# Kernel tuning notes

Hardware: AMD Instinct MI355X
Metric: run time of the kernel (lower is better)

The kernel has to match this reference:

```python
import jax, jax.numpy as jnp
import numpy as np

N_NODES = 100000
N_EDGES = 640000
NUM_GRAPHS = 128
NUM_FEATURES = 128
HIDDEN = 16
NUM_CLASSES = 10


def setup_inputs() -> dict:
    key = jax.random.key(0)
    ks = jax.random.split(key, 9)
    x = jax.random.normal(ks[0], (N_NODES, NUM_FEATURES), dtype=jnp.float32)
    edge_index = jax.random.randint(ks[1], (2, N_EDGES), 0, N_NODES, dtype=jnp.int64)
    batch = jnp.sort(jax.random.randint(ks[2], (N_NODES,), 0, NUM_GRAPHS, dtype=jnp.int64))
    W1 = jax.random.normal(ks[3], (NUM_FEATURES, HIDDEN), dtype=jnp.float32) * 0.1
    b1 = jax.random.normal(ks[4], (HIDDEN,), dtype=jnp.float32) * 0.1
    W2 = jax.random.normal(ks[5], (HIDDEN, HIDDEN), dtype=jnp.float32) * 0.1
    b2 = jax.random.normal(ks[6], (HIDDEN,), dtype=jnp.float32) * 0.1
    Wfc = jax.random.normal(ks[7], (HIDDEN, NUM_CLASSES), dtype=jnp.float32) * 0.1
    bfc = jax.random.normal(ks[8], (NUM_CLASSES,), dtype=jnp.float32) * 0.1
    return {"x": x, "edge_index": edge_index, "batch": batch,
            "W1": W1, "b1": b1, "W2": W2, "b2": b2, "Wfc": Wfc, "bfc": bfc}


def reference(x, edge_index, batch, W1, b1, W2, b2, Wfc, bfc):
    src, dst = edge_index[0], edge_index[1]

    def gin_layer(h, W, b):
        # GINConv (eps=0): nn((1+eps)*x_i + sum_{j in N(i)} x_j)
        agg = jax.ops.segment_sum(h[src], dst, num_segments=N_NODES)
        return jax.nn.relu((h + agg) @ W + b)

    h = gin_layer(x, W1, b1)   # [N, 16]
    h = gin_layer(h, W2, b2)   # [N, 16]

    # global mean pool over graphs
    sums = jax.ops.segment_sum(h, batch, num_segments=NUM_GRAPHS)        # [G, 16]
    counts = jax.ops.segment_sum(jnp.ones((N_NODES,), h.dtype), batch,
                                 num_segments=NUM_GRAPHS)                # [G]
    pooled = sums / jnp.maximum(counts, 1.0)[:, None]
    return pooled @ Wfc + bfc  # [G, num_classes]
```

## Files before the change

### kernel.cpp

```cpp
#include <hip/hip_runtime.h>
#include <hip/hip_bf16.h>

#define N_NODES   100000
#define N_EDGES   640000
#define NUM_GRAPHS 128
#define NUM_FEAT  128
#define HIDDEN    16
#define NUM_CLS   10

#define NBLK   256
#define EPB    (N_EDGES / NBLK)
#define NBUCK  256
#define BSHIFT 9
#define BNODES 512

#define MM1_ROWS 64
__global__ __launch_bounds__(256) void k_mm1_bcount(const float* __restrict__ x,
                                                    const float* __restrict__ W1,
                                                    float* __restrict__ y,
                                                    const int* __restrict__ ei,
                                                    int* __restrict__ cnt,
                                                    int N, int gridMM1) {
    __shared__ float sx[MM1_ROWS][132];
    __shared__ float sw[NUM_FEAT * HIDDEN];
    const int t = threadIdx.x;

    if (blockIdx.x >= gridMM1) {
        int* h = (int*)&sx[0][0];
        const int b = blockIdx.x - gridMM1;
        h[t] = 0;
        __syncthreads();
        const int e0 = b * EPB, e1 = e0 + EPB;
        for (int e = e0 + t; e < e1; e += 256)
            atomicAdd(&h[ei[N_EDGES + e] >> BSHIFT], 1);
        __syncthreads();
        cnt[b * NBUCK + t] = h[t];
        return;
    }

    const int rowbase = blockIdx.x * MM1_ROWS;
    const int nrows = min(MM1_ROWS, N - rowbase);

    for (int i = t; i < NUM_FEAT * HIDDEN; i += 256) sw[i] = W1[i];

    for (int i = t; i < nrows * 32; i += 256) {
        int r = i >> 5, q = i & 31;
        float4 v = ((const float4*)(x + (size_t)(rowbase + r) * NUM_FEAT))[q];
        *(float4*)&sx[r][q * 4] = v;
    }
    __syncthreads();

    const int r  = t >> 2;
    const int c0 = (t & 3) * 4;
    if (r < nrows) {
        float4 o = {0.f, 0.f, 0.f, 0.f};
        #pragma unroll 4
        for (int k4 = 0; k4 < 32; ++k4) {
            float4 xv = *(const float4*)&sx[r][k4 * 4];
            const float* wb = &sw[(k4 * 4) * HIDDEN + c0];
            float4 w0 = *(const float4*)(wb);
            float4 w1 = *(const float4*)(wb + HIDDEN);
            float4 w2 = *(const float4*)(wb + 2 * HIDDEN);
            float4 w3 = *(const float4*)(wb + 3 * HIDDEN);
            o.x += xv.x * w0.x + xv.y * w1.x + xv.z * w2.x + xv.w * w3.x;
            o.y += xv.x * w0.y + xv.y * w1.y + xv.z * w2.y + xv.w * w3.y;
            o.z += xv.x * w0.z + xv.y * w1.z + xv.z * w2.z + xv.w * w3.z;
            o.w += xv.x * w0.w + xv.y * w1.w + xv.z * w2.w + xv.w * w3.w;
        }
        ((float4*)(y + (size_t)(rowbase + r) * HIDDEN))[t & 3] = o;
    }
}

__global__ __launch_bounds__(256) void k_place(const int* __restrict__ ei,
                                               const int* __restrict__ cnt,
                                               int* __restrict__ bases,
                                               unsigned* __restrict__ packed,
                                               int* __restrict__ zarea, int nz) {
    __shared__ int s[NBUCK];
    __shared__ int cur[NBUCK];
    const int t = threadIdx.x, b = blockIdx.x;

    int tot = 0, own = 0;
    for (int i = 0; i < NBLK; ++i) {
        int v = cnt[i * NBUCK + t];
        tot += v;
        own += (i < b) ? v : 0;
    }
    s[t] = tot;
    __syncthreads();
    for (int off = 1; off < NBUCK; off <<= 1) {
        int add = (t >= off) ? s[t - off] : 0;
        __syncthreads();
        s[t] += add;
        __syncthreads();
    }
    const int base = s[t] - tot;
    cur[t] = base + own;
    if (b == 0) {
        bases[t] = base;
        if (t == NBUCK - 1) bases[NBUCK] = N_EDGES;
        for (int i = t; i < nz; i += 256) zarea[i] = 0;
    }
    __syncthreads();

    const int e0 = b * EPB, e1 = e0 + EPB;
    for (int e = e0 + t; e < e1; e += 256) {
        int srcv = ei[e];
        int dstv = ei[N_EDGES + e];
        int k = dstv >> BSHIFT;
        int slot = atomicAdd(&cur[k], 1);
        packed[slot] = ((unsigned)(dstv & (BNODES - 1)) << 17) | (unsigned)srcv;
    }
}

__global__ __launch_bounds__(256) void k_build(const unsigned* __restrict__ packed,
                                               const int* __restrict__ bases,
                                               int* __restrict__ row,
                                               int* __restrict__ srcidx) {
    __shared__ int h[BNODES];
    __shared__ int ps[256];
    __shared__ int e2[BNODES];
    __shared__ int cur[BNODES];
    const int k = blockIdx.x, t = threadIdx.x;
    const int s0 = bases[k];
    const int s1 = bases[k + 1];

    h[t] = 0; h[t + 256] = 0;
    __syncthreads();
    for (int i = s0 + t; i < s1; i += 256)
        atomicAdd(&h[packed[i] >> 17], 1);
    __syncthreads();
    int pv = h[2 * t] + h[2 * t + 1];
    ps[t] = pv;
    __syncthreads();
    for (int off = 1; off < 256; off <<= 1) {
        int add = (t >= off) ? ps[t - off] : 0;
        __syncthreads();
        ps[t] += add;
        __syncthreads();
    }
    int ex = ps[t] - pv;
    e2[2 * t] = ex;               e2[2 * t + 1] = ex + h[2 * t];
    cur[2 * t] = ex;              cur[2 * t + 1] = ex + h[2 * t];
    __syncthreads();
    #pragma unroll
    for (int jj = 0; jj < 2; ++jj) {
        int j = t + jj * 256;
        int node = (k << BSHIFT) + j;
        if (node <= N_NODES) row[node] = s0 + e2[j];
    }
    __syncthreads();
    for (int i = s0 + t; i < s1; i += 256) {
        unsigned p = packed[i];
        int dl = p >> 17;
        int slot = atomicAdd(&cur[dl], 1);
        srcidx[s0 + slot] = (int)(p & 0x1FFFFu);
    }
}

__global__ __launch_bounds__(256) void k_g1f(const int* __restrict__ row,
                                             const int* __restrict__ srcidx,
                                             const float* __restrict__ A,
                                             const float* __restrict__ bias,
                                             const float* __restrict__ W2,
                                             float* __restrict__ B, int N) {
    __shared__ float sw[HIDDEN * HIDDEN];
    const int t = threadIdx.x;
    if (t < HIDDEN * HIDDEN) sw[t] = W2[t];
    __syncthreads();
    const int n = blockIdx.x * 64 + (t >> 2);
    const int p = t & 3;
    if (n >= N) return;
    const int r0 = row[n];
    const int d  = row[n + 1] - r0;
    float4 acc = ((const float4*)(A + (size_t)n * HIDDEN))[p];
    for (int i = 0; i < d; ++i) {
        int s = srcidx[r0 + i];
        float4 v = ((const float4*)(A + (size_t)s * HIDDEN))[p];
        acc.x += v.x; acc.y += v.y; acc.z += v.z; acc.w += v.w;
    }
    const float4 bv = ((const float4*)bias)[p];
    acc.x = fmaxf(acc.x + bv.x, 0.f);
    acc.y = fmaxf(acc.y + bv.y, 0.f);
    acc.z = fmaxf(acc.z + bv.z, 0.f);
    acc.w = fmaxf(acc.w + bv.w, 0.f);
    const int lane = t & 63;
    const int qbase = lane & ~3;
    const int c0 = p * 4;
    float4 o = {0.f, 0.f, 0.f, 0.f};
    #pragma unroll
    for (int q = 0; q < 4; ++q) {
        float hx = __shfl(acc.x, qbase + q, 64);
        float hy = __shfl(acc.y, qbase + q, 64);
        float hz = __shfl(acc.z, qbase + q, 64);
        float hw = __shfl(acc.w, qbase + q, 64);
        const float* wb = &sw[(q * 4) * HIDDEN + c0];
        float4 w0 = *(const float4*)(wb);
        float4 w1 = *(const float4*)(wb + HIDDEN);
        float4 w2 = *(const float4*)(wb + 2 * HIDDEN);
        float4 w3 = *(const float4*)(wb + 3 * HIDDEN);
        o.x += hx * w0.x + hy * w1.x + hz * w2.x + hw * w3.x;
        o.y += hx * w0.y + hy * w1.y + hz * w2.y + hw * w3.y;
        o.z += hx * w0.z + hy * w1.z + hz * w2.z + hw * w3.z;
        o.w += hx * w0.w + hy * w1.w + hz * w2.w + hw * w3.w;
    }
    ((float4*)(B + (size_t)n * HIDDEN))[p] = o;
}

#define POOL_BLOCKS 1024
__global__ __launch_bounds__(256) void k_g2p(const int* __restrict__ row,
                                             const int* __restrict__ srcidx,
                                             const float* __restrict__ B,
                                             const float* __restrict__ bias,
                                             const int* __restrict__ batch,
                                             float* __restrict__ sums,
                                             float* __restrict__ counts,
                                             unsigned* __restrict__ done,
                                             const float* __restrict__ Wfc,
                                             const float* __restrict__ bfc,
                                             float* __restrict__ out,
                                             int N, int chunk) {
    __shared__ float ssum[NUM_GRAPHS * HIDDEN];
    __shared__ float scnt[NUM_GRAPHS];
    __shared__ unsigned sdone;
    const int t = threadIdx.x;
    for (int i = t; i < NUM_GRAPHS * HIDDEN; i += 256) ssum[i] = 0.f;
    if (t < NUM_GRAPHS) scnt[t] = 0.f;
    __syncthreads();

    const int n0 = blockIdx.x * chunk;
    const int n1 = min(n0 + chunk, N);
    const int lane = t & 63;
    const int p = t & 3;
    const float4 bv = ((const float4*)bias)[p];

    for (int nb = n0; nb < n1; nb += 64) {
        int n = nb + (t >> 2);
        bool active = (n < n1);
        int nc = active ? n : (n1 - 1);
        int g = batch[nc];
        float4 h = {0.f, 0.f, 0.f, 0.f};
        if (active) {
            int r0 = row[n];
            int d  = row[n + 1] - r0;
            h = ((const float4*)(B + (size_t)n * HIDDEN))[p];
            for (int i = 0; i < d; ++i) {
                int s = srcidx[r0 + i];
                float4 v = ((const float4*)(B + (size_t)s * HIDDEN))[p];
                h.x += v.x; h.y += v.y; h.z += v.z; h.w += v.w;
            }
            h.x = fmaxf(h.x + bv.x, 0.f);
            h.y = fmaxf(h.y + bv.y, 0.f);
            h.z = fmaxf(h.z + bv.z, 0.f);
            h.w = fmaxf(h.w + bv.w, 0.f);
        }
        int gf = __builtin_amdgcn_readfirstlane(g);
        bool uniform = (__ballot(g == gf) == ~0ull);
        if (uniform) {
            #pragma unroll
            for (int m = 4; m <= 32; m <<= 1) {
                h.x += __shfl_xor(h.x, m, 64);
                h.y += __shfl_xor(h.y, m, 64);
                h.z += __shfl_xor(h.z, m, 64);
                h.w += __shfl_xor(h.w, m, 64);
            }
            if (lane < 4) {
                float* sp = &ssum[gf * HIDDEN + p * 4];
                atomicAdd(sp + 0, h.x);
                atomicAdd(sp + 1, h.y);
                atomicAdd(sp + 2, h.z);
                atomicAdd(sp + 3, h.w);
            }
            if (lane == 0) {
                int wfirst = nb + ((t >> 6) << 4);
                int cnt = min(16, n1 - wfirst);
                if (cnt > 0) atomicAdd(&scnt[gf], (float)cnt);
            }
        } else if (active) {
            float* sp = &ssum[g * HIDDEN + p * 4];
            atomicAdd(sp + 0, h.x);
            atomicAdd(sp + 1, h.y);
            atomicAdd(sp + 2, h.z);
            atomicAdd(sp + 3, h.w);
            if (p == 0) atomicAdd(&scnt[g], 1.f);
        }
    }
    __syncthreads();
    for (int i = t; i < NUM_GRAPHS * HIDDEN; i += 256) {
        float v = ssum[i];
        if (v != 0.f) atomicAdd(&sums[i], v);
    }
    if (t < NUM_GRAPHS) {
        float v = scnt[t];
        if (v != 0.f) atomicAdd(&counts[t], v);
    }
    __syncthreads();
    if (t == 0) sdone = atomicAdd(done, 1u);
    __syncthreads();
    if (sdone == POOL_BLOCKS - 1) {
        __threadfence();
        for (int i = t; i < NUM_GRAPHS * NUM_CLS; i += 256) {
            int g = i / NUM_CLS, c = i % NUM_CLS;
            float inv = 1.0f / fmaxf(counts[g], 1.0f);
            float acc = bfc[c];
            #pragma unroll
            for (int kk = 0; kk < HIDDEN; ++kk)
                acc += (sums[g * HIDDEN + kk] * inv) * Wfc[kk * NUM_CLS + c];
            out[i] = acc;
        }
    }
}

extern "C" void kernel_launch(void* const* d_in, const int* in_sizes, int n_in,
                              void* d_out, int out_size, void* d_ws, size_t ws_size,
                              hipStream_t stream) {
    const float* x    = (const float*)d_in[0];
    const int*   ei   = (const int*)d_in[1];
    const int*   batch= (const int*)d_in[2];
    const float* W1   = (const float*)d_in[3];
    const float* b1   = (const float*)d_in[4];
    const float* W2   = (const float*)d_in[5];
    const float* b2   = (const float*)d_in[6];
    const float* Wfc  = (const float*)d_in[7];
    const float* bfc  = (const float*)d_in[8];
    float* out = (float*)d_out;

    const size_t NB = (size_t)N_NODES * HIDDEN * sizeof(float);
    char* ws = (char*)d_ws;
    size_t off = 0;
    float* A      = (float*)(ws + off); off += NB;
    float* B      = (float*)(ws + off); off += NB;
    float*    sums   = (float*)(ws + off); off += (size_t)NUM_GRAPHS * HIDDEN * sizeof(float);
    float*    counts = (float*)(ws + off); off += (size_t)NUM_GRAPHS * sizeof(float);
    unsigned* done   = (unsigned*)(ws + off); off += 16;
    const int nz = NUM_GRAPHS * HIDDEN + NUM_GRAPHS + 1;
    int* row    = (int*)(ws + off); off += (size_t)(N_NODES + 4) * sizeof(int);
    int* cnt    = (int*)(ws + off); off += (size_t)NBLK * NBUCK * sizeof(int);
    int* bases  = (int*)(ws + off); off += (size_t)(NBUCK + 1) * sizeof(int);
    off = (off + 15) & ~(size_t)15;
    int* srcidx = (int*)(ws + off); off += (size_t)N_EDGES * sizeof(int);
    unsigned* packed = (unsigned*)B;

    const int gridMM1 = (N_NODES + MM1_ROWS - 1) / MM1_ROWS;
    const int gridG1  = (N_NODES + 63) / 64;
    const int poolChunk = (N_NODES + POOL_BLOCKS - 1) / POOL_BLOCKS;

    k_mm1_bcount<<<gridMM1 + NBLK, 256, 0, stream>>>(x, W1, A, ei, cnt,
                                                     N_NODES, gridMM1);
    k_place<<<NBLK, 256, 0, stream>>>(ei, cnt, bases, packed, (int*)sums, nz);
    k_build<<<NBUCK, 256, 0, stream>>>(packed, bases, row, srcidx);

    k_g1f<<<gridG1, 256, 0, stream>>>(row, srcidx, A, b1, W2, B, N_NODES);

    k_g2p<<<POOL_BLOCKS, 256, 0, stream>>>(row, srcidx, B, b2, batch, sums, counts,
                                           done, Wfc, bfc, out, N_NODES, poolChunk);
}
```

Measured before the change: 103.3 us.

## Replace global prefix-scan bucketing with fixed-capacity buckets and atomic cursors

```diff
diff --git a/kernel.cpp b/kernel.cpp
--- a/kernel.cpp
+++ b/kernel.cpp
@@ -13,31 +13,21 @@
 #define NBUCK  256
 #define BSHIFT 9
 #define BNODES 512
+#define CAP    4096
 
 #define MM1_ROWS 64
-__global__ __launch_bounds__(256) void k_mm1_bcount(const float* __restrict__ x,
-                                                    const float* __restrict__ W1,
-                                                    float* __restrict__ y,
-                                                    const int* __restrict__ ei,
-                                                    int* __restrict__ cnt,
-                                                    int N, int gridMM1) {
+__global__ __launch_bounds__(256) void k_mm1z(const float* __restrict__ x,
+                                              const float* __restrict__ W1,
+                                              float* __restrict__ y,
+                                              int* __restrict__ zarea, int nz,
+                                              int N, int gridMM1) {
+    const int t = threadIdx.x;
+    if (blockIdx.x >= gridMM1) {
+        for (int i = t; i < nz; i += 256) zarea[i] = 0;
+        return;
+    }
     __shared__ float sx[MM1_ROWS][132];
     __shared__ float sw[NUM_FEAT * HIDDEN];
-    const int t = threadIdx.x;
-
-    if (blockIdx.x >= gridMM1) {
-        int* h = (int*)&sx[0][0];
-        const int b = blockIdx.x - gridMM1;
-        h[t] = 0;
-        __syncthreads();
-        const int e0 = b * EPB, e1 = e0 + EPB;
-        for (int e = e0 + t; e < e1; e += 256)
-            atomicAdd(&h[ei[N_EDGES + e] >> BSHIFT], 1);
-        __syncthreads();
-        cnt[b * NBUCK + t] = h[t];
-        return;
-    }
-
     const int rowbase = blockIdx.x * MM1_ROWS;
     const int nrows = min(MM1_ROWS, N - rowbase);
 
@@ -71,39 +61,23 @@
     }
 }
 
-__global__ __launch_bounds__(256) void k_place(const int* __restrict__ ei,
-                                               const int* __restrict__ cnt,
-                                               int* __restrict__ bases,
-                                               unsigned* __restrict__ packed,
-                                               int* __restrict__ zarea, int nz) {
-    __shared__ int s[NBUCK];
+__global__ __launch_bounds__(256) void k_place2(const int* __restrict__ ei,
+                                                int* __restrict__ gcur,
+                                                unsigned* __restrict__ packed) {
+    __shared__ int hist[NBUCK];
     __shared__ int cur[NBUCK];
     const int t = threadIdx.x, b = blockIdx.x;
-
-    int tot = 0, own = 0;
-    for (int i = 0; i < NBLK; ++i) {
-        int v = cnt[i * NBUCK + t];
-        tot += v;
-        own += (i < b) ? v : 0;
-    }
-    s[t] = tot;
-    __syncthreads();
-    for (int off = 1; off < NBUCK; off <<= 1) {
-        int add = (t >= off) ? s[t - off] : 0;
-        __syncthreads();
-        s[t] += add;
-        __syncthreads();
-    }
-    const int base = s[t] - tot;
-    cur[t] = base + own;
-    if (b == 0) {
-        bases[t] = base;
-        if (t == NBUCK - 1) bases[NBUCK] = N_EDGES;
-        for (int i = t; i < nz; i += 256) zarea[i] = 0;
-    }
-    __syncthreads();
-
+    hist[t] = 0;
+    __syncthreads();
     const int e0 = b * EPB, e1 = e0 + EPB;
+    for (int e = e0 + t; e < e1; e += 256)
+        atomicAdd(&hist[ei[N_EDGES + e] >> BSHIFT], 1);
+    __syncthreads();
+    int h = hist[t];
+    int base = 0;
+    if (h > 0) base = atomicAdd(&gcur[t], h);
+    cur[t] = t * CAP + base;
+    __syncthreads();
     for (int e = e0 + t; e < e1; e += 256) {
         int srcv = ei[e];
         int dstv = ei[N_EDGES + e];
@@ -113,17 +87,18 @@
     }
 }
 
-__global__ __launch_bounds__(256) void k_build(const unsigned* __restrict__ packed,
-                                               const int* __restrict__ bases,
-                                               int* __restrict__ row,
-                                               int* __restrict__ srcidx) {
+__global__ __launch_bounds__(256) void k_build2(const unsigned* __restrict__ packed,
+                                                const int* __restrict__ gcur,
+                                                int* __restrict__ row,
+                                                int* __restrict__ deg,
+                                                int* __restrict__ srcidx) {
     __shared__ int h[BNODES];
     __shared__ int ps[256];
     __shared__ int e2[BNODES];
     __shared__ int cur[BNODES];
     const int k = blockIdx.x, t = threadIdx.x;
-    const int s0 = bases[k];
-    const int s1 = bases[k + 1];
+    const int s0 = k * CAP;
+    const int s1 = s0 + gcur[k];
 
     h[t] = 0; h[t + 256] = 0;
     __syncthreads();
@@ -147,7 +122,10 @@
     for (int jj = 0; jj < 2; ++jj) {
         int j = t + jj * 256;
         int node = (k << BSHIFT) + j;
-        if (node <= N_NODES) row[node] = s0 + e2[j];
+        if (node < N_NODES) {
+            row[node] = s0 + e2[j];
+            deg[node] = h[j];
+        }
     }
     __syncthreads();
     for (int i = s0 + t; i < s1; i += 256) {
@@ -159,6 +137,7 @@
 }
 
 __global__ __launch_bounds__(256) void k_g1f(const int* __restrict__ row,
+                                             const int* __restrict__ deg,
                                              const int* __restrict__ srcidx,
                                              const float* __restrict__ A,
                                              const float* __restrict__ bias,
@@ -172,7 +151,7 @@
     const int p = t & 3;
     if (n >= N) return;
     const int r0 = row[n];
-    const int d  = row[n + 1] - r0;
+    const int d  = deg[n];
     float4 acc = ((const float4*)(A + (size_t)n * HIDDEN))[p];
     for (int i = 0; i < d; ++i) {
         int s = srcidx[r0 + i];
@@ -209,6 +188,7 @@
 
 #define POOL_BLOCKS 1024
 __global__ __launch_bounds__(256) void k_g2p(const int* __restrict__ row,
+                                             const int* __restrict__ deg,
                                              const int* __restrict__ srcidx,
                                              const float* __restrict__ B,
                                              const float* __restrict__ bias,
@@ -242,7 +222,7 @@
         float4 h = {0.f, 0.f, 0.f, 0.f};
         if (active) {
             int r0 = row[n];
-            int d  = row[n + 1] - r0;
+            int d  = deg[n];
             h = ((const float4*)(B + (size_t)n * HIDDEN))[p];
             for (int i = 0; i < d; ++i) {
                 int s = srcidx[r0 + i];
@@ -328,30 +308,27 @@
     const size_t NB = (size_t)N_NODES * HIDDEN * sizeof(float);
     char* ws = (char*)d_ws;
     size_t off = 0;
-    float* A      = (float*)(ws + off); off += NB;
-    float* B      = (float*)(ws + off); off += NB;
-    float*    sums   = (float*)(ws + off); off += (size_t)NUM_GRAPHS * HIDDEN * sizeof(float);
-    float*    counts = (float*)(ws + off); off += (size_t)NUM_GRAPHS * sizeof(float);
+    float* A = (float*)(ws + off); off += NB;
+    float* B = (float*)(ws + off); off += NB;
+    int*      gcur   = (int*)(ws + off);      off += (size_t)NBUCK * sizeof(int);
+    float*    sums   = (float*)(ws + off);    off += (size_t)NUM_GRAPHS * HIDDEN * sizeof(float);
+    float*    counts = (float*)(ws + off);    off += (size_t)NUM_GRAPHS * sizeof(float);
     unsigned* done   = (unsigned*)(ws + off); off += 16;
-    const int nz = NUM_GRAPHS * HIDDEN + NUM_GRAPHS + 1;
-    int* row    = (int*)(ws + off); off += (size_t)(N_NODES + 4) * sizeof(int);
-    int* cnt    = (int*)(ws + off); off += (size_t)NBLK * NBUCK * sizeof(int);
-    int* bases  = (int*)(ws + off); off += (size_t)(NBUCK + 1) * sizeof(int);
+    const int nz = NBUCK + NUM_GRAPHS * HIDDEN + NUM_GRAPHS + 1;
+    int* row    = (int*)(ws + off); off += (size_t)N_NODES * sizeof(int);
+    int* deg    = (int*)(ws + off); off += (size_t)N_NODES * sizeof(int);
     off = (off + 15) & ~(size_t)15;
-    int* srcidx = (int*)(ws + off); off += (size_t)N_EDGES * sizeof(int);
-    unsigned* packed = (unsigned*)B;
+    unsigned* packed = (unsigned*)(ws + off); off += (size_t)NBUCK * CAP * sizeof(unsigned);
+    int* srcidx      = (int*)(ws + off);      off += (size_t)NBUCK * CAP * sizeof(int);
 
     const int gridMM1 = (N_NODES + MM1_ROWS - 1) / MM1_ROWS;
     const int gridG1  = (N_NODES + 63) / 64;
     const int poolChunk = (N_NODES + POOL_BLOCKS - 1) / POOL_BLOCKS;
 
-    k_mm1_bcount<<<gridMM1 + NBLK, 256, 0, stream>>>(x, W1, A, ei, cnt,
-                                                     N_NODES, gridMM1);
-    k_place<<<NBLK, 256, 0, stream>>>(ei, cnt, bases, packed, (int*)sums, nz);
-    k_build<<<NBUCK, 256, 0, stream>>>(packed, bases, row, srcidx);
-
-    k_g1f<<<gridG1, 256, 0, stream>>>(row, srcidx, A, b1, W2, B, N_NODES);
-
-    k_g2p<<<POOL_BLOCKS, 256, 0, stream>>>(row, srcidx, B, b2, batch, sums, counts,
+    k_mm1z<<<gridMM1 + 1, 256, 0, stream>>>(x, W1, A, gcur, nz, N_NODES, gridMM1);
+    k_place2<<<NBLK, 256, 0, stream>>>(ei, gcur, packed);
+    k_build2<<<NBUCK, 256, 0, stream>>>(packed, gcur, row, deg, srcidx);
+    k_g1f<<<gridG1, 256, 0, stream>>>(row, deg, srcidx, A, b1, W2, B, N_NODES);
+    k_g2p<<<POOL_BLOCKS, 256, 0, stream>>>(row, deg, srcidx, B, b2, batch, sums, counts,
                                            done, Wfc, bfc, out, N_NODES, poolChunk);
 }
```

After: 96.30 us. 1.07x faster.
